# Performance work log

Measured on AMD Instinct MI355X. Metric: run time of the kernel, lower is better.

The kernel has to match this reference:

```python
import jax, jax.numpy as jnp
import numpy as np

B, T, S, H = 8, 256, 256, 512

def setup_inputs() -> dict:
    key = jax.random.key(0)
    k1, k2, k3, k4, k5, k6 = jax.random.split(key, 6)
    query = jax.random.normal(k1, (B, T, H), dtype=jnp.float32)
    encoder_outputs = jax.random.normal(k2, (B, S, H), dtype=jnp.float32)
    # lengths in [1, S] so every row has at least one valid source position
    src_lengths = jax.random.randint(k3, (B,), 1, S + 1, dtype=jnp.int64)
    scale = 1.0 / np.sqrt(H)
    W_h = jax.random.normal(k4, (H, H), dtype=jnp.float32) * scale  # nn.Linear weight (out, in)
    W_s = jax.random.normal(k5, (H, H), dtype=jnp.float32) * scale
    v = jax.random.normal(k6, (H,), dtype=jnp.float32) * scale     # nn.Linear(H,1) weight squeezed
    return {"query": query, "encoder_outputs": encoder_outputs,
            "src_lengths": src_lengths, "W_h": W_h, "W_s": W_s, "v": v}

def reference(query, encoder_outputs, src_lengths, W_h, W_s, v):
    # Linear without bias: y = x @ W^T
    enc_f = jnp.einsum('bsh,oh->bso', encoder_outputs, W_h)   # (B,S,H)
    qry_f = jnp.einsum('bth,oh->bto', query, W_s)             # (B,T,H)
    # additive score: v^T tanh(enc_f + qry_f), broadcast over (T,S)
    scores = jnp.einsum('btsh,h->bts',
                        jnp.tanh(enc_f[:, None, :, :] + qry_f[:, :, None, :]), v)  # (B,T,S)
    mask = jnp.arange(S)[None, :] >= src_lengths[:, None]      # (B,S) True = pad
    scores = jnp.where(mask[:, None, :], -jnp.inf, scores)
    attn_weights = jax.nn.softmax(scores, axis=-1)             # (B,T,S)
    attn_out = jnp.einsum('bts,bsh->bth', attn_weights, encoder_outputs)
    return attn_out
```

## Files before the change

### kernel.cpp

```cpp
#include <hip/hip_runtime.h>
#include <hip/hip_cooperative_groups.h>
#include <cstddef>
#include <math.h>

namespace cg = cooperative_groups;

#define BD 8
#define TD 256
#define SD 256
#define HD 512
#define K2F 2.885390081777927f

#define EXP2(x) __builtin_amdgcn_exp2f(x)
#define RCP(x)  __builtin_amdgcn_rcpf(x)

typedef __attribute__((ext_vector_type(8))) _Float16 half8;
typedef __attribute__((ext_vector_type(4))) _Float16 half4;
typedef __attribute__((ext_vector_type(4))) float float4v;

__device__ __forceinline__ float exp2_sat(float x) {
    return EXP2(fminf(fmaxf(x, -80.0f), 80.0f));
}

#define LSTR 40

__device__ __forceinline__ void phaseA(
    int bid, int tid, float* smem,
    const float* __restrict__ enc, const float* __restrict__ qry,
    const float* __restrict__ Wh,  const float* __restrict__ Ws,
    float* __restrict__ encT, float* __restrict__ qryf)
{
    const int l  = tid & 63;
    const int w  = tid >> 6;
    const int rf = l & 15;
    const int q  = l >> 4;

    _Float16* LA = (_Float16*)smem;
    _Float16* LB = (_Float16*)(smem + 1280);

    const int x  = bid & 7;
    const int k  = bid >> 3;
    const bool isq = k >= 32;
    const int kk = k & 31;
    const int my = (isq ? 32 : 0) + x * 4 + (kk & 3);
    const int n0 = (kk >> 2) * 64;
    const int m0 = my * 64;

    const int srow = tid >> 3;
    const int scol = (tid & 7) * 4;
    const float* Abase = isq
        ? qry + (size_t)(m0 - 2048 + srow) * HD + scol
        : enc + (size_t)(m0 + srow) * HD + scol;
    const float* Bbase = (isq ? Ws : Wh) + (size_t)(n0 + srow) * HD + scol;

    const int mi = (w & 3) * 16;
    const int ni = (w >> 2) * 32;

    float4v acc[2] = {{0,0,0,0},{0,0,0,0}};

    float4 a0 = *(const float4*)(Abase);
    float4 b0 = *(const float4*)(Bbase);

    for (int ks = 0; ks < 16; ++ks) {
        if (ks) __syncthreads();
        {
            half4 ha, hb;
            ha[0]=(_Float16)a0.x; ha[1]=(_Float16)a0.y; ha[2]=(_Float16)a0.z; ha[3]=(_Float16)a0.w;
            hb[0]=(_Float16)b0.x; hb[1]=(_Float16)b0.y; hb[2]=(_Float16)b0.z; hb[3]=(_Float16)b0.w;
            *(half4*)&LA[srow * LSTR + scol] = ha;
            *(half4*)&LB[srow * LSTR + scol] = hb;
        }
        __syncthreads();
        if (ks + 1 < 16) {
            const int ko = (ks + 1) * 32;
            a0 = *(const float4*)(Abase + ko);
            b0 = *(const float4*)(Bbase + ko);
        }
        half8 ah = *(const half8*)&LA[(mi + rf) * LSTR + q * 8];
        #pragma unroll
        for (int j = 0; j < 2; ++j) {
            half8 bh = *(const half8*)&LB[(ni + j * 16 + rf) * LSTR + q * 8];
            acc[j] = __builtin_amdgcn_mfma_f32_16x16x32_f16(ah, bh, acc[j], 0, 0, 0);
        }
    }

    if (!isq) {
        const int b  = m0 >> 8;
        const int sb = (m0 & 255) + mi + q * 4;
        float* base = encT + (size_t)b * HD * SD;
        #pragma unroll
        for (int j = 0; j < 2; ++j) {
            float4 o = make_float4(exp2_sat(acc[j][0]*K2F), exp2_sat(acc[j][1]*K2F),
                                   exp2_sat(acc[j][2]*K2F), exp2_sat(acc[j][3]*K2F));
            *(float4*)(base + (size_t)(n0 + ni + j * 16 + rf) * SD + sb) = o;
        }
    } else {
        const int mrow = (m0 - 2048) + mi + q * 4;
        #pragma unroll
        for (int j = 0; j < 2; ++j)
            #pragma unroll
            for (int r = 0; r < 4; ++r)
                qryf[(size_t)(mrow + r) * HD + n0 + ni + j * 16 + rf] =
                    exp2_sat(acc[j][r] * K2F);
    }
}

__device__ __forceinline__ void phaseA1024(
    int bid, int tid, float* smem,
    const float* __restrict__ enc, const float* __restrict__ qry,
    const float* __restrict__ Wh,  const float* __restrict__ Ws,
    float* __restrict__ encT, float* __restrict__ qryf)
{
    const int l  = tid & 63;
    const int w  = tid >> 6;
    const int rf = l & 15;
    const int q  = l >> 4;

    _Float16* LA = (_Float16*)smem;
    _Float16* LB = (_Float16*)(smem + 1280);

    const int x  = bid & 7;
    const int k  = bid >> 3;
    const bool isq = k >= 32;
    const int kk = k & 31;
    const int my = (isq ? 32 : 0) + x * 4 + (kk & 3);
    const int n0 = (kk >> 2) * 64;
    const int m0 = my * 64;

    const bool stagesA = (tid < 512);
    const int srow = (tid >> 3) & 63;
    const int scol = (tid & 7) * 4;
    const float* Sbase = stagesA
        ? (isq ? qry + (size_t)(m0 - 2048 + srow) * HD
               : enc + (size_t)(m0 + srow) * HD) + scol
        : (isq ? Ws : Wh) + (size_t)(n0 + srow) * HD + scol;
    _Float16* Ldst = (stagesA ? LA : LB) + srow * LSTR + scol;

    const int mi = (w & 3) * 16;
    const int ni = (w >> 2) * 16;

    float4v acc = {0, 0, 0, 0};

    float4 a0 = *(const float4*)(Sbase);

    for (int ks = 0; ks < 16; ++ks) {
        if (ks) __syncthreads();
        {
            half4 ha;
            ha[0]=(_Float16)a0.x; ha[1]=(_Float16)a0.y; ha[2]=(_Float16)a0.z; ha[3]=(_Float16)a0.w;
            *(half4*)Ldst = ha;
        }
        __syncthreads();
        if (ks + 1 < 16) a0 = *(const float4*)(Sbase + (ks + 1) * 32);
        half8 ah = *(const half8*)&LA[(mi + rf) * LSTR + q * 8];
        half8 bh = *(const half8*)&LB[(ni + rf) * LSTR + q * 8];
        acc = __builtin_amdgcn_mfma_f32_16x16x32_f16(ah, bh, acc, 0, 0, 0);
    }

    if (!isq) {
        const int b  = m0 >> 8;
        const int sb = (m0 & 255) + mi + q * 4;
        float* base = encT + (size_t)b * HD * SD;
        float4 o = make_float4(exp2_sat(acc[0]*K2F), exp2_sat(acc[1]*K2F),
                               exp2_sat(acc[2]*K2F), exp2_sat(acc[3]*K2F));
        *(float4*)(base + (size_t)(n0 + ni + rf) * SD + sb) = o;
    } else {
        const int mrow = (m0 - 2048) + mi + q * 4;
        #pragma unroll
        for (int r = 0; r < 4; ++r)
            qryf[(size_t)(mrow + r) * HD + n0 + ni + rf] = exp2_sat(acc[r] * K2F);
    }
}

template<int TT>
__device__ __forceinline__ void phaseB(
    int b, int t0, int tid, float* smem,
    const float* __restrict__ enc, const float* __restrict__ encT,
    const float* __restrict__ qryf, const float* __restrict__ v,
    const int* __restrict__ lens, float* __restrict__ out)
{
    const int l = tid & 63;
    const int w = tid >> 6;

    float* qls = smem;
    float* pls = smem + 512 * TT;
    float* wls = smem + 1536 * TT;

    {
        const float* qf = qryf + ((size_t)b * TD + t0) * HD;
        #pragma unroll
        for (int t = 0; t < TT; ++t) qls[tid * TT + t] = qf[t * HD + tid];
    }
    __syncthreads();

    float a[TT][4];
    #pragma unroll
    for (int t = 0; t < TT; ++t)
        #pragma unroll
        for (int c = 0; c < 4; ++c) a[t][c] = 0.0f;
    {
        const float* ep = encT + (size_t)b * HD * SD + (size_t)(w * 64) * SD + l * 4;
        const int jbase = w * 64;
        #pragma unroll 4
        for (int jj = 0; jj < 64; ++jj) {
            float4 e = *(const float4*)(ep + (size_t)jj * SD);
            float vj = v[jbase + jj];
            float qv[TT];
            #pragma unroll
            for (int t = 0; t < TT; ++t) qv[t] = qls[(jbase + jj) * TT + t];
            float ev[4] = {e.x, e.y, e.z, e.w};
            #pragma unroll
            for (int t = 0; t < TT; ++t)
                #pragma unroll
                for (int c = 0; c < 4; ++c) {
                    float p = fmaf(ev[c], qv[t], 1.0f);
                    a[t][c] = fmaf(vj, RCP(p), a[t][c]);
                }
        }
    }
    if (w < 4) {
        #pragma unroll
        for (int t = 0; t < TT; ++t)
            *(float4*)&pls[(w * TT + t) * 256 + l * 4] =
                make_float4(a[t][0], a[t][1], a[t][2], a[t][3]);
    }
    __syncthreads();
    if (w >= 4) {
        #pragma unroll
        for (int t = 0; t < TT; ++t) {
            float4 c4 = *(const float4*)&pls[((w - 4) * TT + t) * 256 + l * 4];
            c4.x += a[t][0]; c4.y += a[t][1]; c4.z += a[t][2]; c4.w += a[t][3];
            *(float4*)&pls[((w - 4) * TT + t) * 256 + l * 4] = c4;
        }
    }
    __syncthreads();

    if (w < TT) {
        const int t = w;
        float p[4] = {0, 0, 0, 0};
        #pragma unroll
        for (int g = 0; g < 4; ++g) {
            float4 pp = *(const float4*)&pls[(g * TT + t) * 256 + l * 4];
            p[0] += pp.x; p[1] += pp.y; p[2] += pp.z; p[3] += pp.w;
        }
        const int len = lens[b];
        const int s0 = l * 4;
        float sc[4];
        #pragma unroll
        for (int c = 0; c < 4; ++c)
            sc[c] = (s0 + c < len) ? -2.0f * p[c] : -INFINITY;
        float mx = fmaxf(fmaxf(sc[0], sc[1]), fmaxf(sc[2], sc[3]));
        #pragma unroll
        for (int off = 32; off; off >>= 1) mx = fmaxf(mx, __shfl_xor(mx, off));
        float ex[4]; float sum = 0.0f;
        #pragma unroll
        for (int c = 0; c < 4; ++c) { ex[c] = __expf(sc[c] - mx); sum += ex[c]; }
        #pragma unroll
        for (int off = 32; off; off >>= 1) sum += __shfl_xor(sum, off);
        const float inv = RCP(sum);
        *(float4*)&wls[t * SD + s0] = make_float4(ex[0]*inv, ex[1]*inv, ex[2]*inv, ex[3]*inv);
    }
    __syncthreads();

    const int sg = tid >> 7;
    const int h4 = (tid & 127) * 4;
    float* avred = pls;
    float4 o[TT];
    #pragma unroll
    for (int t = 0; t < TT; ++t) o[t] = make_float4(0.f, 0.f, 0.f, 0.f);
    {
        const float* eb = enc + (size_t)b * SD * HD + h4;
        #pragma unroll 2
        for (int ss = 0; ss < 64; ++ss) {
            const int s = sg * 64 + ss;
            float4 evv = *(const float4*)(eb + (size_t)s * HD);
            float wt[TT];
            #pragma unroll
            for (int t = 0; t < TT; ++t) wt[t] = wls[t * SD + s];
            #pragma unroll
            for (int t = 0; t < TT; ++t) {
                o[t].x = fmaf(wt[t], evv.x, o[t].x);
                o[t].y = fmaf(wt[t], evv.y, o[t].y);
                o[t].z = fmaf(wt[t], evv.z, o[t].z);
                o[t].w = fmaf(wt[t], evv.w, o[t].w);
            }
        }
    }
    if (sg < 2) {
        #pragma unroll
        for (int t = 0; t < TT; ++t)
            *(float4*)&avred[(size_t)(sg * TT + t) * 512 + h4] = o[t];
    }
    __syncthreads();
    if (sg >= 2) {
        #pragma unroll
        for (int t = 0; t < TT; ++t) {
            float4 c4 = *(const float4*)&avred[(size_t)((sg - 2) * TT + t) * 512 + h4];
            c4.x += o[t].x; c4.y += o[t].y; c4.z += o[t].z; c4.w += o[t].w;
            *(float4*)&avred[(size_t)((sg - 2) * TT + t) * 512 + h4] = c4;
        }
    }
    __syncthreads();

    if (tid < TT * 128) {
        const int t  = tid >> 7;
        const int hh = (tid & 127) * 4;
        float4 x0 = *(const float4*)&avred[(size_t)(0 * TT + t) * 512 + hh];
        float4 x1 = *(const float4*)&avred[(size_t)(1 * TT + t) * 512 + hh];
        float4 r = make_float4(x0.x + x1.x, x0.y + x1.y, x0.z + x1.z, x0.w + x1.w);
        *(float4*)(out + ((size_t)b * TD + t0 + t) * HD + hh) = r;
    }
}

__device__ __forceinline__ void phaseB1024(
    int b, int t0, int tid, float* smem,
    const float* __restrict__ enc, const float* __restrict__ encT,
    const float* __restrict__ qryf, const float* __restrict__ v,
    const int* __restrict__ lens, float* __restrict__ out)
{
    const int l = tid & 63;
    const int w = tid >> 6;

    float* qls = smem;
    float* pls = smem + 4096;
    float* wls = smem + 12288;

    {
        const float* qf = qryf + ((size_t)b * TD + t0) * HD;
        const int j = tid & 511;
        #pragma unroll
        for (int t = (tid >> 9); t < 8; t += 2)
            qls[t * 512 + j] = qf[t * HD + j];
    }
    __syncthreads();

    float a[8][4];
    #pragma unroll
    for (int t = 0; t < 8; ++t)
        #pragma unroll
        for (int c = 0; c < 4; ++c) a[t][c] = 0.0f;
    {
        const int jbase = w * 32;
        const float* ep = encT + (size_t)b * HD * SD + (size_t)jbase * SD + l * 4;
        #pragma unroll 4
        for (int jj = 0; jj < 32; ++jj) {
            float4 e = *(const float4*)(ep + (size_t)jj * SD);
            float vj = v[jbase + jj];
            float qv[8];
            #pragma unroll
            for (int t = 0; t < 8; ++t) qv[t] = qls[t * 512 + jbase + jj];
            float ev[4] = {e.x, e.y, e.z, e.w};
            #pragma unroll
            for (int t = 0; t < 8; ++t)
                #pragma unroll
                for (int c = 0; c < 4; ++c) {
                    float p = fmaf(ev[c], qv[t], 1.0f);
                    a[t][c] = fmaf(vj, RCP(p), a[t][c]);
                }
        }
    }
    if (w < 4) {
        #pragma unroll
        for (int t = 0; t < 8; ++t)
            *(float4*)&pls[(w * 8 + t) * 256 + l * 4] =
                make_float4(a[t][0], a[t][1], a[t][2], a[t][3]);
    }
    __syncthreads();
    if (w >= 4 && w < 8) {
        #pragma unroll
        for (int t = 0; t < 8; ++t) {
            float4 c4 = *(const float4*)&pls[((w - 4) * 8 + t) * 256 + l * 4];
            c4.x += a[t][0]; c4.y += a[t][1]; c4.z += a[t][2]; c4.w += a[t][3];
            *(float4*)&pls[((w - 4) * 8 + t) * 256 + l * 4] = c4;
        }
    }
    __syncthreads();
    if (w >= 8 && w < 12) {
        #pragma unroll
        for (int t = 0; t < 8; ++t) {
            float4 c4 = *(const float4*)&pls[((w - 8) * 8 + t) * 256 + l * 4];
            c4.x += a[t][0]; c4.y += a[t][1]; c4.z += a[t][2]; c4.w += a[t][3];
            *(float4*)&pls[((w - 8) * 8 + t) * 256 + l * 4] = c4;
        }
    }
    __syncthreads();
    if (w >= 12) {
        #pragma unroll
        for (int t = 0; t < 8; ++t) {
            float4 c4 = *(const float4*)&pls[((w - 12) * 8 + t) * 256 + l * 4];
            c4.x += a[t][0]; c4.y += a[t][1]; c4.z += a[t][2]; c4.w += a[t][3];
            *(float4*)&pls[((w - 12) * 8 + t) * 256 + l * 4] = c4;
        }
    }
    __syncthreads();

    if (w < 8) {
        const int t = w;
        float p[4] = {0, 0, 0, 0};
        #pragma unroll
        for (int g = 0; g < 4; ++g) {
            float4 pp = *(const float4*)&pls[(g * 8 + t) * 256 + l * 4];
            p[0] += pp.x; p[1] += pp.y; p[2] += pp.z; p[3] += pp.w;
        }
        const int len = lens[b];
        const int s0 = l * 4;
        float sc[4];
        #pragma unroll
        for (int c = 0; c < 4; ++c)
            sc[c] = (s0 + c < len) ? -2.0f * p[c] : -INFINITY;
        float mx = fmaxf(fmaxf(sc[0], sc[1]), fmaxf(sc[2], sc[3]));
        #pragma unroll
        for (int off = 32; off; off >>= 1) mx = fmaxf(mx, __shfl_xor(mx, off));
        float ex[4]; float sum = 0.0f;
        #pragma unroll
        for (int c = 0; c < 4; ++c) { ex[c] = __expf(sc[c] - mx); sum += ex[c]; }
        #pragma unroll
        for (int off = 32; off; off >>= 1) sum += __shfl_xor(sum, off);
        const float inv = RCP(sum);
        *(float4*)&wls[t * SD + s0] = make_float4(ex[0]*inv, ex[1]*inv, ex[2]*inv, ex[3]*inv);
    }
    __syncthreads();

    const int sg = tid >> 7;
    const int h4 = (tid & 127) * 4;
    float* avred = pls;
    float4 o[8];
    #pragma unroll
    for (int t = 0; t < 8; ++t) o[t] = make_float4(0.f, 0.f, 0.f, 0.f);
    {
        const float* eb = enc + (size_t)b * SD * HD + h4;
        #pragma unroll 2
        for (int ss = 0; ss < 32; ++ss) {
            const int s = sg * 32 + ss;
            float4 evv = *(const float4*)(eb + (size_t)s * HD);
            float wt[8];
            #pragma unroll
            for (int t = 0; t < 8; ++t) wt[t] = wls[t * SD + s];
            #pragma unroll
            for (int t = 0; t < 8; ++t) {
                o[t].x = fmaf(wt[t], evv.x, o[t].x);
                o[t].y = fmaf(wt[t], evv.y, o[t].y);
                o[t].z = fmaf(wt[t], evv.z, o[t].z);
                o[t].w = fmaf(wt[t], evv.w, o[t].w);
            }
        }
    }
    if (sg < 2) {
        #pragma unroll
        for (int t = 0; t < 8; ++t)
            *(float4*)&avred[(size_t)(sg * 8 + t) * 512 + h4] = o[t];
    }
    __syncthreads();
    if (sg >= 2 && sg < 4) {
        #pragma unroll
        for (int t = 0; t < 8; ++t) {
            float4 c4 = *(const float4*)&avred[(size_t)((sg - 2) * 8 + t) * 512 + h4];
            c4.x += o[t].x; c4.y += o[t].y; c4.z += o[t].z; c4.w += o[t].w;
            *(float4*)&avred[(size_t)((sg - 2) * 8 + t) * 512 + h4] = c4;
        }
    }
    __syncthreads();
    if (sg >= 4 && sg < 6) {
        #pragma unroll
        for (int t = 0; t < 8; ++t) {
            float4 c4 = *(const float4*)&avred[(size_t)((sg - 4) * 8 + t) * 512 + h4];
            c4.x += o[t].x; c4.y += o[t].y; c4.z += o[t].z; c4.w += o[t].w;
            *(float4*)&avred[(size_t)((sg - 4) * 8 + t) * 512 + h4] = c4;
        }
    }
    __syncthreads();
    if (sg >= 6) {
        #pragma unroll
        for (int t = 0; t < 8; ++t) {
            float4 c4 = *(const float4*)&avred[(size_t)((sg - 6) * 8 + t) * 512 + h4];
            c4.x += o[t].x; c4.y += o[t].y; c4.z += o[t].z; c4.w += o[t].w;
            *(float4*)&avred[(size_t)((sg - 6) * 8 + t) * 512 + h4] = c4;
        }
    }
    __syncthreads();

    {
        const int t  = tid >> 7;
        const int hh = (tid & 127) * 4;
        float4 x0 = *(const float4*)&avred[(size_t)(0 * 8 + t) * 512 + hh];
        float4 x1 = *(const float4*)&avred[(size_t)(1 * 8 + t) * 512 + hh];
        float4 r = make_float4(x0.x + x1.x, x0.y + x1.y, x0.z + x1.z, x0.w + x1.w);
        *(float4*)(out + ((size_t)b * TD + t0 + t) * HD + hh) = r;
    }
}

__global__ __launch_bounds__(1024, 4) void fusedW(
    const float* __restrict__ enc, const float* __restrict__ qry,
    const float* __restrict__ Wh,  const float* __restrict__ Ws,
    const float* __restrict__ v,   const int* __restrict__ lens,
    float* __restrict__ encT, float* __restrict__ qryf, float* __restrict__ out)
{
    __shared__ float smem[14336];
    const int bid = blockIdx.x;
    const int tid = threadIdx.x;

    phaseA1024(bid, tid, smem, enc, qry, Wh, Ws, encT, qryf);
    __syncthreads();
    phaseA1024(bid + 256, tid, smem, enc, qry, Wh, Ws, encT, qryf);

    cg::this_grid().sync();

    phaseB1024(bid & 7, (bid >> 3) * 8, tid, smem, enc, encT, qryf, v, lens, out);
}

__global__ __launch_bounds__(512) void fused512(
    const float* __restrict__ enc, const float* __restrict__ qry,
    const float* __restrict__ Wh,  const float* __restrict__ Ws,
    const float* __restrict__ v,   const int* __restrict__ lens,
    float* __restrict__ encT, float* __restrict__ qryf, float* __restrict__ out)
{
    __shared__ float smem[7168];
    const int bid = blockIdx.x;
    phaseA(bid, threadIdx.x, smem, enc, qry, Wh, Ws, encT, qryf);
    cg::this_grid().sync();
    phaseB<4>(bid & 7, (bid >> 3) * 4, threadIdx.x, smem,
              enc, encT, qryf, v, lens, out);
}

__global__ __launch_bounds__(256) void proj_fb(
    const float* __restrict__ enc, const float* __restrict__ qry,
    const float* __restrict__ Wh,  const float* __restrict__ Ws,
    float* __restrict__ encT, float* __restrict__ qryf)
{
    __shared__ _Float16 LA[64 * LSTR], LB[64 * LSTR];

    const int tid = threadIdx.x;
    const int l = tid & 63, w = tid >> 6;
    const int rf = l & 15, q = l >> 4;
    const int my = blockIdx.y;
    const bool isq = my >= 32;
    const int m0 = my * 64;
    const int n0 = blockIdx.x * 64;

    const int srow = tid >> 2;
    const int scol = (tid & 3) * 8;
    const float* Abase = isq
        ? qry + (size_t)(m0 - 2048 + srow) * HD + scol
        : enc + (size_t)(m0 + srow) * HD + scol;
    const float* Bbase = (isq ? Ws : Wh) + (size_t)(n0 + srow) * HD + scol;

    const int mi = (w & 1) * 32, ni = (w >> 1) * 32;
    float4v acc[2][2] = {{{0,0,0,0},{0,0,0,0}},{{0,0,0,0},{0,0,0,0}}};

    float4 a0 = *(const float4*)(Abase);
    float4 a1 = *(const float4*)(Abase + 4);
    float4 b0 = *(const float4*)(Bbase);
    float4 b1 = *(const float4*)(Bbase + 4);

    for (int ks = 0; ks < 16; ++ks) {
        if (ks) __syncthreads();
        {
            float af[8] = {a0.x,a0.y,a0.z,a0.w,a1.x,a1.y,a1.z,a1.w};
            float bf[8] = {b0.x,b0.y,b0.z,b0.w,b1.x,b1.y,b1.z,b1.w};
            half8 ha, hb;
            #pragma unroll
            for (int i = 0; i < 8; ++i) { ha[i] = (_Float16)af[i]; hb[i] = (_Float16)bf[i]; }
            *(half8*)&LA[srow * LSTR + scol] = ha;
            *(half8*)&LB[srow * LSTR + scol] = hb;
        }
        __syncthreads();
        if (ks + 1 < 16) {
            const int ko = (ks + 1) * 32;
            a0 = *(const float4*)(Abase + ko);
            a1 = *(const float4*)(Abase + ko + 4);
            b0 = *(const float4*)(Bbase + ko);
            b1 = *(const float4*)(Bbase + ko + 4);
        }
        half8 ah[2], bh[2];
        #pragma unroll
        for (int i = 0; i < 2; ++i) {
            ah[i] = *(const half8*)&LA[(mi + i * 16 + rf) * LSTR + q * 8];
            bh[i] = *(const half8*)&LB[(ni + i * 16 + rf) * LSTR + q * 8];
        }
        #pragma unroll
        for (int i = 0; i < 2; ++i)
            #pragma unroll
            for (int j = 0; j < 2; ++j)
                acc[i][j] = __builtin_amdgcn_mfma_f32_16x16x32_f16(ah[i], bh[j], acc[i][j], 0, 0, 0);
    }

    if (!isq) {
        const int b  = m0 >> 8;
        const int sb = (m0 & 255) + mi + q * 4;
        float* base = encT + (size_t)b * HD * SD;
        #pragma unroll
        for (int i = 0; i < 2; ++i)
            #pragma unroll
            for (int j = 0; j < 2; ++j) {
                float4 o = make_float4(exp2_sat(acc[i][j][0]*K2F), exp2_sat(acc[i][j][1]*K2F),
                                       exp2_sat(acc[i][j][2]*K2F), exp2_sat(acc[i][j][3]*K2F));
                *(float4*)(base + (size_t)(n0 + ni + j * 16 + rf) * SD + sb + i * 16) = o;
            }
    } else {
        const int mrow = (m0 - 2048) + mi + q * 4;
        #pragma unroll
        for (int i = 0; i < 2; ++i)
            #pragma unroll
            for (int j = 0; j < 2; ++j)
                #pragma unroll
                for (int r = 0; r < 4; ++r)
                    qryf[(size_t)(mrow + i * 16 + r) * HD + n0 + ni + j * 16 + rf] =
                        exp2_sat(acc[i][j][r] * K2F);
    }
}

__global__ __launch_bounds__(512) void attn_fb(
    const float* __restrict__ enc, const float* __restrict__ encT,
    const float* __restrict__ qryf, const float* __restrict__ v,
    const int* __restrict__ lens, float* __restrict__ out)
{
    __shared__ float qls[HD * 4];
    __shared__ float pls[8 * 4 * 256];
    __shared__ float wls[4 * SD];

    const int blk = blockIdx.x;
    const int b   = blk >> 6;
    const int t0  = (blk & 63) * 4;
    const int tid = threadIdx.x;
    const int w   = tid >> 6;
    const int l   = tid & 63;

    {
        const float* qf = qryf + ((size_t)b * TD + t0) * HD;
        float4 qv;
        qv.x = qf[0 * HD + tid]; qv.y = qf[1 * HD + tid];
        qv.z = qf[2 * HD + tid]; qv.w = qf[3 * HD + tid];
        *(float4*)&qls[tid * 4] = qv;
    }
    __syncthreads();

    float a[4][4];
    #pragma unroll
    for (int t = 0; t < 4; ++t)
        #pragma unroll
        for (int c = 0; c < 4; ++c) a[t][c] = 0.0f;
    {
        const float* ep = encT + (size_t)b * HD * SD + (size_t)(w * 64) * SD + l * 4;
        const int jbase = w * 64;
        #pragma unroll 4
        for (int jj = 0; jj < 64; ++jj) {
            float4 e = *(const float4*)(ep + (size_t)jj * SD);
            float4 q4 = *(const float4*)&qls[(jbase + jj) * 4];
            float vj = v[jbase + jj];
            float ev[4] = {e.x, e.y, e.z, e.w};
            float qv[4] = {q4.x, q4.y, q4.z, q4.w};
            #pragma unroll
            for (int t = 0; t < 4; ++t)
                #pragma unroll
                for (int c = 0; c < 4; ++c) {
                    float p = fmaf(ev[c], qv[t], 1.0f);
                    a[t][c] = fmaf(vj, RCP(p), a[t][c]);
                }
        }
    }
    #pragma unroll
    for (int t = 0; t < 4; ++t)
        *(float4*)&pls[(w * 4 + t) * 256 + l * 4] = make_float4(a[t][0], a[t][1], a[t][2], a[t][3]);
    __syncthreads();

    if (w < 4) {
        const int t = w;
        float p[4] = {0, 0, 0, 0};
        #pragma unroll
        for (int g = 0; g < 8; ++g) {
            float4 pp = *(const float4*)&pls[(g * 4 + t) * 256 + l * 4];
            p[0] += pp.x; p[1] += pp.y; p[2] += pp.z; p[3] += pp.w;
        }
        const int len = lens[b];
        const int s0 = l * 4;
        float sc[4];
        #pragma unroll
        for (int c = 0; c < 4; ++c)
            sc[c] = (s0 + c < len) ? -2.0f * p[c] : -INFINITY;
        float mx = fmaxf(fmaxf(sc[0], sc[1]), fmaxf(sc[2], sc[3]));
        #pragma unroll
        for (int off = 32; off; off >>= 1) mx = fmaxf(mx, __shfl_xor(mx, off));
        float ex[4]; float sum = 0.0f;
        #pragma unroll
        for (int c = 0; c < 4; ++c) { ex[c] = __expf(sc[c] - mx); sum += ex[c]; }
        #pragma unroll
        for (int off = 32; off; off >>= 1) sum += __shfl_xor(sum, off);
        const float inv = RCP(sum);
        *(float4*)&wls[t * SD + s0] = make_float4(ex[0]*inv, ex[1]*inv, ex[2]*inv, ex[3]*inv);
    }
    __syncthreads();

    const int g  = tid >> 7;
    const int h4 = (tid & 127) * 4;
    float* avred = pls;
    {
        const float* eb = enc + (size_t)b * SD * HD + h4;
        float4 o[4] = {{0,0,0,0},{0,0,0,0},{0,0,0,0},{0,0,0,0}};
        #pragma unroll 2
        for (int ss = 0; ss < 64; ++ss) {
            const int s = g * 64 + ss;
            float4 evv = *(const float4*)(eb + (size_t)s * HD);
            float wt[4];
            #pragma unroll
            for (int t = 0; t < 4; ++t) wt[t] = wls[t * SD + s];
            #pragma unroll
            for (int t = 0; t < 4; ++t) {
                o[t].x = fmaf(wt[t], evv.x, o[t].x);
                o[t].y = fmaf(wt[t], evv.y, o[t].y);
                o[t].z = fmaf(wt[t], evv.z, o[t].z);
                o[t].w = fmaf(wt[t], evv.w, o[t].w);
            }
        }
        #pragma unroll
        for (int t = 0; t < 4; ++t)
            *(float4*)&avred[(size_t)(g * 4 + t) * 512 + h4] = o[t];
    }
    __syncthreads();
    {
        const int t  = tid >> 7;
        const int hh = (tid & 127) * 4;
        float4 r = {0, 0, 0, 0};
        #pragma unroll
        for (int gg = 0; gg < 4; ++gg) {
            float4 x = *(const float4*)&avred[(size_t)(gg * 4 + t) * 512 + hh];
            r.x += x.x; r.y += x.y; r.z += x.z; r.w += x.w;
        }
        *(float4*)(out + ((size_t)b * TD + t0 + t) * HD + hh) = r;
    }
}

extern "C" void kernel_launch(void* const* d_in, const int* in_sizes, int n_in,
                              void* d_out, int out_size, void* d_ws, size_t ws_size,
                              hipStream_t stream) {
    const float* query = (const float*)d_in[0];
    const float* enc   = (const float*)d_in[1];
    const int*   lens  = (const int*)d_in[2];
    const float* W_h   = (const float*)d_in[3];
    const float* W_s   = (const float*)d_in[4];
    const float* v     = (const float*)d_in[5];
    float* out = (float*)d_out;

    char* ws = (char*)d_ws;
    float* encT = (float*)(ws);
    float* qryf = (float*)(ws + ((size_t)4 << 20));

    void* args[] = {
        (void*)&enc, (void*)&query, (void*)&W_h, (void*)&W_s,
        (void*)&v, (void*)&lens, (void*)&encT, (void*)&qryf, (void*)&out
    };

    int nb = 0;
    hipError_t oerr = hipOccupancyMaxActiveBlocksPerMultiprocessor(
        &nb, (const void*)fusedW, 1024, 0);
    if (oerr == hipSuccess && nb >= 1) {
        hipError_t lerr = hipLaunchCooperativeKernel((const void*)fusedW,
                                                     dim3(256), dim3(1024), args, 0, stream);
        if (lerr == hipSuccess) return;
    }

    nb = 0;
    oerr = hipOccupancyMaxActiveBlocksPerMultiprocessor(
        &nb, (const void*)fused512, 512, 0);
    if (oerr == hipSuccess && nb >= 2) {
        hipError_t lerr = hipLaunchCooperativeKernel((const void*)fused512,
                                                     dim3(512), dim3(512), args, 0, stream);
        if (lerr == hipSuccess) return;
    }

    dim3 pgrid(HD / 64, 64);
    proj_fb<<<pgrid, 256, 0, stream>>>(enc, query, W_h, W_s, encT, qryf);
    attn_fb<<<BD * (TD / 4), 512, 0, stream>>>(enc, encT, qryf, v, lens, out);
}
```

Measured before the change: 121.1 us.

## Add fp32 reciprocal-based score phase variant and launch it first

Adds a new attention phase (phaseB1024X) and a cooperative kernel fusedX that uses it. The phase uses the identity tanh(x+y) = 1 - 2/(1+e^{2x}e^{2y}) on exponentiated projections, so each score term becomes one FMA plus one fp32 reciprocal, with the constant term dropped because softmax ignores it. The weighted sum over encoder rows and the cross-wave reductions go through LDS. fusedX is tried before the existing fusedW path. The per-element fp32 reciprocal may cost more than the previous path's arithmetic if that path used packed half math.

After: 121.0 us. No clear change (-0.1%).

```diff
diff --git a/kernel.cpp b/kernel.cpp
--- a/kernel.cpp
+++ b/kernel.cpp
@@ -312,6 +312,196 @@
     }
 }
 
+__device__ __forceinline__ void phaseB1024X(
+    int b, int t0, int tid, float* smem,
+    const float* __restrict__ enc, const float* __restrict__ encT,
+    const float* __restrict__ qryf, const float* __restrict__ v,
+    const int* __restrict__ lens, float* __restrict__ out)
+{
+    const int l = tid & 63;
+    const int w = tid >> 6;
+
+    float* qls = smem;
+    float* pls = smem + 4096;
+    float* wls = smem + 12288;
+
+    {
+        const float* qf = qryf + ((size_t)b * TD + t0) * HD;
+        const int j = tid & 511;
+        #pragma unroll
+        for (int t = (tid >> 9); t < 8; t += 2)
+            qls[t * 512 + j] = qf[t * HD + j];
+    }
+    __syncthreads();
+
+    float a[8][4];
+    #pragma unroll
+    for (int t = 0; t < 8; ++t)
+        #pragma unroll
+        for (int c = 0; c < 4; ++c) a[t][c] = 0.0f;
+    {
+        const int jbase = w * 32;
+        const float* ep = encT + (size_t)b * HD * SD + (size_t)jbase * SD + l * 4;
+        #pragma unroll 1
+        for (int j0 = 0; j0 < 32; j0 += 8) {
+            float4 e8[8];
+            #pragma unroll
+            for (int u = 0; u < 8; ++u)
+                e8[u] = *(const float4*)(ep + (size_t)(j0 + u) * SD);
+            #pragma unroll
+            for (int u = 0; u < 8; ++u) {
+                const int jj = j0 + u;
+                const float vj = v[jbase + jj];
+                float qv[8];
+                #pragma unroll
+                for (int t = 0; t < 8; ++t) qv[t] = qls[t * 512 + jbase + jj];
+                float ev[4] = {e8[u].x, e8[u].y, e8[u].z, e8[u].w};
+                #pragma unroll
+                for (int t = 0; t < 8; ++t)
+                    #pragma unroll
+                    for (int c = 0; c < 4; ++c) {
+                        float p = fmaf(ev[c], qv[t], 1.0f);
+                        a[t][c] = fmaf(vj, RCP(p), a[t][c]);
+                    }
+            }
+        }
+    }
+    if (w < 4) {
+        #pragma unroll
+        for (int t = 0; t < 8; ++t)
+            *(float4*)&pls[(w * 8 + t) * 256 + l * 4] =
+                make_float4(a[t][0], a[t][1], a[t][2], a[t][3]);
+    }
+    __syncthreads();
+    if (w >= 4 && w < 8) {
+        #pragma unroll
+        for (int t = 0; t < 8; ++t) {
+            float4 c4 = *(const float4*)&pls[((w - 4) * 8 + t) * 256 + l * 4];
+            c4.x += a[t][0]; c4.y += a[t][1]; c4.z += a[t][2]; c4.w += a[t][3];
+            *(float4*)&pls[((w - 4) * 8 + t) * 256 + l * 4] = c4;
+        }
+    }
+    __syncthreads();
+    if (w >= 8 && w < 12) {
+        #pragma unroll
+        for (int t = 0; t < 8; ++t) {
+            float4 c4 = *(const float4*)&pls[((w - 8) * 8 + t) * 256 + l * 4];
+            c4.x += a[t][0]; c4.y += a[t][1]; c4.z += a[t][2]; c4.w += a[t][3];
+            *(float4*)&pls[((w - 8) * 8 + t) * 256 + l * 4] = c4;
+        }
+    }
+    __syncthreads();
+    if (w >= 12) {
+        #pragma unroll
+        for (int t = 0; t < 8; ++t) {
+            float4 c4 = *(const float4*)&pls[((w - 12) * 8 + t) * 256 + l * 4];
+            c4.x += a[t][0]; c4.y += a[t][1]; c4.z += a[t][2]; c4.w += a[t][3];
+            *(float4*)&pls[((w - 12) * 8 + t) * 256 + l * 4] = c4;
+        }
+    }
+    __syncthreads();
+
+    if (w < 8) {
+        const int t = w;
+        float p[4] = {0, 0, 0, 0};
+        #pragma unroll
+        for (int g = 0; g < 4; ++g) {
+            float4 pp = *(const float4*)&pls[(g * 8 + t) * 256 + l * 4];
+            p[0] += pp.x; p[1] += pp.y; p[2] += pp.z; p[3] += pp.w;
+        }
+        const int len = lens[b];
+        const int s0 = l * 4;
+        float sc[4];
+        #pragma unroll
+        for (int c = 0; c < 4; ++c)
+            sc[c] = (s0 + c < len) ? -2.0f * p[c] : -INFINITY;
+        float mx = fmaxf(fmaxf(sc[0], sc[1]), fmaxf(sc[2], sc[3]));
+        #pragma unroll
+        for (int off = 32; off; off >>= 1) mx = fmaxf(mx, __shfl_xor(mx, off));
+        float ex[4]; float sum = 0.0f;
+        #pragma unroll
+        for (int c = 0; c < 4; ++c) { ex[c] = __expf(sc[c] - mx); sum += ex[c]; }
+        #pragma unroll
+        for (int off = 32; off; off >>= 1) sum += __shfl_xor(sum, off);
+        const float inv = RCP(sum);
+        *(float4*)&wls[t * SD + s0] = make_float4(ex[0]*inv, ex[1]*inv, ex[2]*inv, ex[3]*inv);
+    }
+    __syncthreads();
+
+    const int sg = tid >> 7;
+    const int h4 = (tid & 127) * 4;
+    float* avred = pls;
+    float4 o[8];
+    #pragma unroll
+    for (int t = 0; t < 8; ++t) o[t] = make_float4(0.f, 0.f, 0.f, 0.f);
+    {
+        const float* eb = enc + (size_t)b * SD * HD + h4;
+        #pragma unroll 1
+        for (int s0b = 0; s0b < 32; s0b += 8) {
+            float4 ev8[8];
+            #pragma unroll
+            for (int u = 0; u < 8; ++u)
+                ev8[u] = *(const float4*)(eb + (size_t)(sg * 32 + s0b + u) * HD);
+            #pragma unroll
+            for (int u = 0; u < 8; ++u) {
+                const int s = sg * 32 + s0b + u;
+                float wt[8];
+                #pragma unroll
+                for (int t = 0; t < 8; ++t) wt[t] = wls[t * SD + s];
+                #pragma unroll
+                for (int t = 0; t < 8; ++t) {
+                    o[t].x = fmaf(wt[t], ev8[u].x, o[t].x);
+                    o[t].y = fmaf(wt[t], ev8[u].y, o[t].y);
+                    o[t].z = fmaf(wt[t], ev8[u].z, o[t].z);
+                    o[t].w = fmaf(wt[t], ev8[u].w, o[t].w);
+                }
+            }
+        }
+    }
+    if (sg < 2) {
+        #pragma unroll
+        for (int t = 0; t < 8; ++t)
+            *(float4*)&avred[(size_t)(sg * 8 + t) * 512 + h4] = o[t];
+    }
+    __syncthreads();
+    if (sg >= 2 && sg < 4) {
+        #pragma unroll
+        for (int t = 0; t < 8; ++t) {
+            float4 c4 = *(const float4*)&avred[(size_t)((sg - 2) * 8 + t) * 512 + h4];
+            c4.x += o[t].x; c4.y += o[t].y; c4.z += o[t].z; c4.w += o[t].w;
+            *(float4*)&avred[(size_t)((sg - 2) * 8 + t) * 512 + h4] = c4;
+        }
+    }
+    __syncthreads();
+    if (sg >= 4 && sg < 6) {
+        #pragma unroll
+        for (int t = 0; t < 8; ++t) {
+            float4 c4 = *(const float4*)&avred[(size_t)((sg - 4) * 8 + t) * 512 + h4];
+            c4.x += o[t].x; c4.y += o[t].y; c4.z += o[t].z; c4.w += o[t].w;
+            *(float4*)&avred[(size_t)((sg - 4) * 8 + t) * 512 + h4] = c4;
+        }
+    }
+    __syncthreads();
+    if (sg >= 6) {
+        #pragma unroll
+        for (int t = 0; t < 8; ++t) {
+            float4 c4 = *(const float4*)&avred[(size_t)((sg - 6) * 8 + t) * 512 + h4];
+            c4.x += o[t].x; c4.y += o[t].y; c4.z += o[t].z; c4.w += o[t].w;
+            *(float4*)&avred[(size_t)((sg - 6) * 8 + t) * 512 + h4] = c4;
+        }
+    }
+    __syncthreads();
+
+    {
+        const int t  = tid >> 7;
+        const int hh = (tid & 127) * 4;
+        float4 x0 = *(const float4*)&avred[(size_t)(0 * 8 + t) * 512 + hh];
+        float4 x1 = *(const float4*)&avred[(size_t)(1 * 8 + t) * 512 + hh];
+        float4 r = make_float4(x0.x + x1.x, x0.y + x1.y, x0.z + x1.z, x0.w + x1.w);
+        *(float4*)(out + ((size_t)b * TD + t0 + t) * HD + hh) = r;
+    }
+}
+
 __device__ __forceinline__ void phaseB1024(
     int b, int t0, int tid, float* smem,
     const float* __restrict__ enc, const float* __restrict__ encT,
@@ -487,6 +677,25 @@
         float4 r = make_float4(x0.x + x1.x, x0.y + x1.y, x0.z + x1.z, x0.w + x1.w);
         *(float4*)(out + ((size_t)b * TD + t0 + t) * HD + hh) = r;
     }
+}
+
+__global__ __launch_bounds__(1024, 4) void fusedX(
+    const float* __restrict__ enc, const float* __restrict__ qry,
+    const float* __restrict__ Wh,  const float* __restrict__ Ws,
+    const float* __restrict__ v,   const int* __restrict__ lens,
+    float* __restrict__ encT, float* __restrict__ qryf, float* __restrict__ out)
+{
+    __shared__ float smem[14336];
+    const int bid = blockIdx.x;
+    const int tid = threadIdx.x;
+
+    phaseA1024(bid, tid, smem, enc, qry, Wh, Ws, encT, qryf);
+    __syncthreads();
+    phaseA1024(bid + 256, tid, smem, enc, qry, Wh, Ws, encT, qryf);
+
+    cg::this_grid().sync();
+
+    phaseB1024X(bid & 7, (bid >> 3) * 8, tid, smem, enc, encT, qryf, v, lens, out);
 }
 
 __global__ __launch_bounds__(1024, 4) void fusedW(
@@ -751,6 +960,15 @@
 
     int nb = 0;
     hipError_t oerr = hipOccupancyMaxActiveBlocksPerMultiprocessor(
+        &nb, (const void*)fusedX, 1024, 0);
+    if (oerr == hipSuccess && nb >= 1) {
+        hipError_t lerr = hipLaunchCooperativeKernel((const void*)fusedX,
+                                                     dim3(256), dim3(1024), args, 0, stream);
+        if (lerr == hipSuccess) return;
+    }
+
+    nb = 0;
+    oerr = hipOccupancyMaxActiveBlocksPerMultiprocessor(
         &nb, (const void*)fusedW, 1024, 0);
     if (oerr == hipSuccess && nb >= 1) {
         hipError_t lerr = hipLaunchCooperativeKernel((const void*)fusedW,
```
